# Kernel tuning notes

Measured on AMD Instinct MI355X. Metric: run time of the kernel, lower is better.

Reference implementation:

```python
import jax, jax.numpy as jnp
from jax import lax
import numpy as np

B, T, H, E = 4096, 16, 1024, 1024


def setup_inputs() -> dict:
    key = jax.random.key(0)
    ks = jax.random.split(key, 6)
    query = jax.random.normal(ks[0], (B, H), dtype=jnp.float32)
    topics = jax.random.normal(ks[1], (B, T, E), dtype=jnp.float32)
    coverage_vector = jax.random.uniform(ks[2], (B, T), dtype=jnp.float32)
    # Ua: Linear(embed->hidden, bias=False); weight [H, E]
    Ua_w = jax.random.normal(ks[3], (H, E), dtype=jnp.float32) * 0.03
    # Wa: Linear(hidden->hidden, bias=False). Applied repeatedly (T times) to
    # query in the original loop, so keep spectral norm < 1 for stability.
    Wa_w = jax.random.normal(ks[4], (H, H), dtype=jnp.float32) * 0.01
    # va: Linear(hidden->1, bias=True)
    va_w = jax.random.normal(ks[5], (1, H), dtype=jnp.float32) * 0.03
    va_b = jnp.zeros((1,), dtype=jnp.float32)
    return {"query": query, "topics": topics, "coverage_vector": coverage_vector,
            "Ua_w": Ua_w, "Wa_w": Wa_w, "va_w": va_w, "va_b": va_b}


def reference(query, topics, coverage_vector, Ua_w, Wa_w, va_w, va_b):
    # proj_key for all steps at once: Ua(topics[:, i, :]) -> [B, T, H]
    proj_keys = jnp.einsum('bte,he->bth', topics, Ua_w)
    # Original loop mutates query = Wa(query) each step, so step i uses
    # Wa^(i+1) @ query. Sequential dependence -> lax.scan over T.
    def step(q, pk_c):
        pk, c = pk_c                       # pk: [B, H], c: [B]
        q = q @ Wa_w.T                     # query = Wa(query)
        s = (jnp.tanh(q + pk) @ va_w.T)[:, 0] + va_b[0]  # va(tanh(.)) -> [B]
        return q, s * c                    # scale by coverage C_t[:, i]
    xs = (jnp.swapaxes(proj_keys, 0, 1), coverage_vector.T)  # [T,B,H], [T,B]
    _, scores = lax.scan(step, query, xs)  # scores: [T, B]
    scores = scores.T                      # [B, T]
    alphas = jax.nn.softmax(scores, axis=1)
    mt = jnp.einsum('bt,bte->be', alphas, topics)  # bmm(alphas[:,None,:], topics)
    return mt, alphas
```

## Files before the change

kernel.cpp:

```cpp
#include <hip/hip_runtime.h>

typedef unsigned short u16;
typedef unsigned int u32;
typedef __attribute__((ext_vector_type(8))) __bf16 bf16x8;
typedef __attribute__((ext_vector_type(4))) float f32x4;

__device__ __forceinline__ u16 f2bf(float f) {
  u32 u = __float_as_uint(f);
  u32 r = (u + 0x7FFFu + ((u >> 16) & 1u)) >> 16;
  return (u16)r;
}

__device__ __forceinline__ void gload_lds16(const void* g, void* l) {
  __builtin_amdgcn_global_load_lds((const __attribute__((address_space(1))) u32*)g,
                                   (__attribute__((address_space(3))) u32*)l, 16, 0, 0);
}

__device__ __forceinline__ float fast_tanh(float x) {
  x = fminf(fmaxf(x, -15.f), 15.f);
  float e2 = __expf(2.f * x);
  return (e2 - 1.f) / (e2 + 1.f);
}

__global__ __launch_bounds__(256) void cvt_kernel(const float* __restrict__ src,
                                                  u16* __restrict__ dst, int n4) {
  int stride = gridDim.x * blockDim.x;
  for (int i = blockIdx.x * blockDim.x + threadIdx.x; i < n4; i += stride) {
    float4 v = reinterpret_cast<const float4*>(src)[i];
    ushort4 o;
    o.x = f2bf(v.x); o.y = f2bf(v.y); o.z = f2bf(v.z); o.w = f2bf(v.w);
    reinterpret_cast<ushort4*>(dst)[i] = o;
  }
}

__global__ __launch_bounds__(256) void cvt3_kernel(const float* __restrict__ q_src, u16* __restrict__ q_dst,
                                                   const float* __restrict__ u_src, u16* __restrict__ u_dst,
                                                   const float* __restrict__ w_src, u16* __restrict__ w_dst) {
  int b = blockIdx.x;
  const float* src; u16* dst; int i;
  if (b < 4096)      { src = q_src; dst = q_dst; i = b * 256 + threadIdx.x; }
  else if (b < 5120) { src = u_src; dst = u_dst; i = (b - 4096) * 256 + threadIdx.x; }
  else               { src = w_src; dst = w_dst; i = (b - 5120) * 256 + threadIdx.x; }
  float4 v = reinterpret_cast<const float4*>(src)[i];
  ushort4 o;
  o.x = f2bf(v.x); o.y = f2bf(v.y); o.z = f2bf(v.z); o.w = f2bf(v.w);
  reinterpret_cast<ushort4*>(dst)[i] = o;
}

__global__ __launch_bounds__(256) void transpose_bf16_kernel(const float* __restrict__ src,
                                                             u16* __restrict__ dst) {
  __shared__ float tile[32][33];
  int tx = threadIdx.x & 31, ty = threadIdx.x >> 5;
  int bx = blockIdx.x * 32, by = blockIdx.y * 32;
#pragma unroll
  for (int j = 0; j < 32; j += 8)
    tile[ty + j][tx] = src[(size_t)(by + ty + j) * 1024 + bx + tx];
  __syncthreads();
#pragma unroll
  for (int j = 0; j < 32; j += 8)
    dst[(size_t)(bx + ty + j) * 1024 + by + tx] = f2bf(tile[tx][ty + j]);
}

__device__ __forceinline__ void stage_tile(const u16* __restrict__ g, size_t row_stride,
                                           u16* lds, int tid) {
#pragma unroll
  for (int s = 0; s < 4; ++s) {
    int chunk = s * 256 + tid;
    int row = chunk >> 3;
    int kcl = (chunk & 7) ^ (row & 7);
    const u16* gp = g + (size_t)row * row_stride + (size_t)(kcl * 8);
    u16* lp = lds + (tid >> 6) * 512 + s * 2048;
    gload_lds16(gp, lp);
  }
}

struct PowArgs {
  const u16* A[8];
  const u16* Bt[8];
  u16* C[8];
  u16* Ct[8];
};

__global__ __launch_bounds__(256) void pow_gemm_kernel(PowArgs args) {
  const u16* A  = args.A[blockIdx.z];
  const u16* Bt = args.Bt[blockIdx.z];
  u16* C  = args.C[blockIdx.z];
  u16* Ct = args.Ct[blockIdx.z];

  __shared__ __align__(16) u16 As[8192];
  __shared__ __align__(16) u16 Bs[8192];

  int tid = threadIdx.x;
  int lane = tid & 63, wave = tid >> 6;
  int wr = wave >> 1, wc = wave & 1;
  int lr = lane & 15, lg = lane >> 4;
  int m0 = blockIdx.x * 128, n0 = blockIdx.y * 128;

  f32x4 acc[4][4];
  const f32x4 zero = {0.f, 0.f, 0.f, 0.f};
#pragma unroll
  for (int m = 0; m < 4; ++m)
#pragma unroll
    for (int n = 0; n < 4; ++n) acc[m][n] = zero;

  for (int k0 = 0; k0 < 1024; k0 += 64) {
    stage_tile(A + (size_t)m0 * 1024 + k0, 1024, As, tid);
    stage_tile(Bt + (size_t)n0 * 1024 + k0, 1024, Bs, tid);
    __syncthreads();
#pragma unroll
    for (int ks = 0; ks < 2; ++ks) {
      bf16x8 a[4], b[4];
#pragma unroll
      for (int m = 0; m < 4; ++m) {
        int ra = wr * 64 + m * 16 + lr;
        a[m] = *reinterpret_cast<const bf16x8*>(As + ra * 64 + (((ks * 4 + lg) ^ (ra & 7)) << 3));
      }
#pragma unroll
      for (int n = 0; n < 4; ++n) {
        int rb = wc * 64 + n * 16 + lr;
        b[n] = *reinterpret_cast<const bf16x8*>(Bs + rb * 64 + (((ks * 4 + lg) ^ (rb & 7)) << 3));
      }
#pragma unroll
      for (int m = 0; m < 4; ++m)
#pragma unroll
        for (int n = 0; n < 4; ++n)
          acc[m][n] = __builtin_amdgcn_mfma_f32_16x16x32_bf16(a[m], b[n], acc[m][n], 0, 0, 0);
    }
    __syncthreads();
  }

#pragma unroll
  for (int m = 0; m < 4; ++m) {
    int row0 = m0 + wr * 64 + m * 16 + lg * 4;
#pragma unroll
    for (int n = 0; n < 4; ++n) {
      int col = n0 + wc * 64 + n * 16 + lr;
      f32x4 c = acc[m][n];
      ushort4 pk;
      pk.x = f2bf(c[0]); pk.y = f2bf(c[1]); pk.z = f2bf(c[2]); pk.w = f2bf(c[3]);
      C[(size_t)(row0 + 0) * 1024 + col] = pk.x;
      C[(size_t)(row0 + 1) * 1024 + col] = pk.y;
      C[(size_t)(row0 + 2) * 1024 + col] = pk.z;
      C[(size_t)(row0 + 3) * 1024 + col] = pk.w;
      *reinterpret_cast<ushort4*>(Ct + (size_t)col * 1024 + row0) = pk;
    }
  }
}

__device__ __forceinline__ void stage_tile64(const u16* __restrict__ g, u16* lds, int tid) {
#pragma unroll
  for (int s = 0; s < 2; ++s) {
    int chunk = s * 256 + tid;
    int row = chunk >> 3;
    int kcl = (chunk & 7) ^ (row & 7);
    const u16* gp = g + (size_t)row * 1024 + (size_t)(kcl * 8);
    u16* lp = lds + (tid >> 6) * 512 + s * 2048;
    gload_lds16(gp, lp);
  }
}

__global__ __launch_bounds__(256) void pow64_gemm_kernel(PowArgs args) {
  const u16* A  = args.A[blockIdx.z];
  const u16* Bt = args.Bt[blockIdx.z];
  u16* C  = args.C[blockIdx.z];
  u16* Ct = args.Ct[blockIdx.z];

  __shared__ __align__(16) u16 As[4096];
  __shared__ __align__(16) u16 Bs[4096];

  int tid = threadIdx.x;
  int lane = tid & 63, wave = tid >> 6;
  int wr = wave >> 1, wc = wave & 1;
  int lr = lane & 15, lg = lane >> 4;
  int m0 = blockIdx.x * 64, n0 = blockIdx.y * 64;

  f32x4 acc[2][2];
  const f32x4 zero = {0.f, 0.f, 0.f, 0.f};
#pragma unroll
  for (int m = 0; m < 2; ++m)
#pragma unroll
    for (int n = 0; n < 2; ++n) acc[m][n] = zero;

  for (int k0 = 0; k0 < 1024; k0 += 64) {
    stage_tile64(A + (size_t)m0 * 1024 + k0, As, tid);
    stage_tile64(Bt + (size_t)n0 * 1024 + k0, Bs, tid);
    __syncthreads();
#pragma unroll
    for (int ks = 0; ks < 2; ++ks) {
      bf16x8 a[2], b[2];
#pragma unroll
      for (int m = 0; m < 2; ++m) {
        int ra = wr * 32 + m * 16 + lr;
        a[m] = *reinterpret_cast<const bf16x8*>(As + ra * 64 + (((ks * 4 + lg) ^ (ra & 7)) << 3));
      }
#pragma unroll
      for (int n = 0; n < 2; ++n) {
        int rb = wc * 32 + n * 16 + lr;
        b[n] = *reinterpret_cast<const bf16x8*>(Bs + rb * 64 + (((ks * 4 + lg) ^ (rb & 7)) << 3));
      }
#pragma unroll
      for (int m = 0; m < 2; ++m)
#pragma unroll
        for (int n = 0; n < 2; ++n)
          acc[m][n] = __builtin_amdgcn_mfma_f32_16x16x32_bf16(a[m], b[n], acc[m][n], 0, 0, 0);
    }
    __syncthreads();
  }

#pragma unroll
  for (int m = 0; m < 2; ++m) {
    int row0 = m0 + wr * 32 + m * 16 + lg * 4;
#pragma unroll
    for (int n = 0; n < 2; ++n) {
      int col = n0 + wc * 32 + n * 16 + lr;
      f32x4 c = acc[m][n];
      ushort4 pk;
      pk.x = f2bf(c[0]); pk.y = f2bf(c[1]); pk.z = f2bf(c[2]); pk.w = f2bf(c[3]);
      C[(size_t)(row0 + 0) * 1024 + col] = pk.x;
      C[(size_t)(row0 + 1) * 1024 + col] = pk.y;
      C[(size_t)(row0 + 2) * 1024 + col] = pk.z;
      C[(size_t)(row0 + 3) * 1024 + col] = pk.w;
      *reinterpret_cast<ushort4*>(Ct + (size_t)col * 1024 + row0) = pk;
    }
  }
}


#define PHASE_READS(CUR, KS, MH)                                                     \
  { _Pragma("unroll") for (int i_ = 0; i_ < 4; ++i_)                                 \
      af[i_] = *reinterpret_cast<const bf16x8*>(lds + aoffv[(MH)*4 + i_] +           \
                                                (CUR)*32768 + (KS)*16384);           \
    if ((MH) == 0) { _Pragma("unroll") for (int n_ = 0; n_ < 4; ++n_)                \
      bfr[n_] = *reinterpret_cast<const bf16x8*>(lds + boffv[n_] +                   \
                                                 (CUR)*32768 + (KS)*16384); } }

#define PHASE_MFMA(MH)                                                               \
  { __builtin_amdgcn_s_barrier();                                                    \
    asm volatile("s_waitcnt lgkmcnt(0)" ::: "memory");                               \
    __builtin_amdgcn_sched_barrier(0);                                               \
    __builtin_amdgcn_s_setprio(1);                                                   \
    _Pragma("unroll") for (int i_ = 0; i_ < 4; ++i_)                                 \
      _Pragma("unroll") for (int n_ = 0; n_ < 4; ++n_)                               \
        acc[(MH)*4 + i_][n_] =                                                       \
            __builtin_amdgcn_mfma_f32_16x16x32_bf16(af[i_], bfr[n_], acc[(MH)*4 + i_][n_], 0, 0, 0); \
    __builtin_amdgcn_s_setprio(0); }

#define PHASE_END()                                                                  \
  { __builtin_amdgcn_s_barrier(); __builtin_amdgcn_sched_barrier(0); }

__global__ __launch_bounds__(512, 2) void score8_kernel(
    const u16* __restrict__ query_bf, const u16* __restrict__ topics_bf,
    const u16* __restrict__ F_base, const u16* __restrict__ Ua_bf,
    const float* __restrict__ va_w, float* __restrict__ scores_raw) {
  extern __shared__ __align__(16) char lds[];

  const int tid = threadIdx.x;
  const int lane = tid & 63, wave = tid >> 6;
  const int wm = wave >> 2, wn = wave & 3;
  const int lr = lane & 15, lg = lane >> 4;
  const int m0 = blockIdx.x * 256, n0 = blockIdx.y * 256;
  const int t = blockIdx.z;
  const int NT = 32;

  const u16* Ft = F_base + (size_t)t * (1024 * 1024);

  u32 aoffv[8], boffv[4];
#pragma unroll
  for (int m = 0; m < 8; ++m) {
    int row = wm * 128 + m * 16 + lr;
    aoffv[m] = row * 64 + ((lg ^ ((row >> 1) & 3)) << 4);
  }
#pragma unroll
  for (int n = 0; n < 4; ++n) {
    int row = wn * 64 + n * 16 + lr;
    boffv[n] = 65536 + row * 64 + ((lg ^ ((row >> 1) & 3)) << 4);
  }

  u32 goff1[2], goff2[2];
#pragma unroll
  for (int s = 0; s < 2; ++s) {
    int c = s * 512 + tid;
    int row = c >> 2;
    int cl = (c & 3) ^ ((row >> 1) & 3);
    goff1[s] = row * 1024 + cl * 8;
    goff2[s] = row * 16384 + cl * 8;
  }
  char* sdst = lds + (tid >> 6) * 1024;
  const u16* qbase = query_bf + (size_t)m0 * 1024;
  const u16* tbase = topics_bf + (size_t)m0 * 16384 + (size_t)t * 1024 - 1024;
  const u16* fbase = Ft + (size_t)n0 * 1024;
  const u16* ubase = Ua_bf + (size_t)n0 * 1024 - 1024;

  auto stageA = [&](int kt, int ks, int buf) {
    const u16* base = (kt < 16 ? qbase : tbase) + kt * 64 + ks * 32;
#pragma unroll
    for (int s = 0; s < 2; ++s) {
      u32 off = (kt < 16) ? goff1[s] : goff2[s];
      gload_lds16(base + off, sdst + buf * 32768 + ks * 16384 + s * 8192);
    }
  };
  auto stageB = [&](int kt, int ks, int buf) {
    const u16* base = (kt < 16 ? fbase : ubase) + kt * 64 + ks * 32;
#pragma unroll
    for (int s = 0; s < 2; ++s)
      gload_lds16(base + goff1[s], sdst + 65536 + buf * 32768 + ks * 16384 + s * 8192);
  };

  f32x4 acc[8][4];
  const f32x4 zero = {0.f, 0.f, 0.f, 0.f};
#pragma unroll
  for (int m = 0; m < 8; ++m)
#pragma unroll
    for (int n = 0; n < 4; ++n) acc[m][n] = zero;

  bf16x8 af[4], bfr[4];

  stageA(0, 0, 0); stageB(0, 0, 0);
  stageA(0, 1, 0); stageB(0, 1, 0);
  stageA(1, 0, 1); stageB(1, 0, 1);
  asm volatile("s_waitcnt vmcnt(4)" ::: "memory");
  __builtin_amdgcn_s_barrier();
  __builtin_amdgcn_sched_barrier(0);

#pragma unroll 2
  for (int kt = 0; kt < NT; ++kt) {
    int cur = kt & 1, nxt = cur ^ 1;
    PHASE_READS(cur, 0, 0);
    if (kt + 1 < NT) stageA(kt + 1, 1, nxt);
    PHASE_MFMA(0); PHASE_END();
    PHASE_READS(cur, 0, 1);
    if (kt + 1 < NT) stageB(kt + 1, 1, nxt);
    PHASE_MFMA(1); PHASE_END();
    PHASE_READS(cur, 1, 0);
    if (kt + 2 < NT) stageA(kt + 2, 0, cur);
    PHASE_MFMA(0); PHASE_END();
    PHASE_READS(cur, 1, 1);
    if (kt + 2 < NT) stageB(kt + 2, 0, cur);
    PHASE_MFMA(1);
    if (kt < NT - 2)       { asm volatile("s_waitcnt vmcnt(4)" ::: "memory"); }
    else if (kt == NT - 2) { asm volatile("s_waitcnt vmcnt(0)" ::: "memory"); }
    PHASE_END();
  }

  float va_c[4];
#pragma unroll
  for (int n = 0; n < 4; ++n) va_c[n] = va_w[n0 + wn * 64 + n * 16 + lr];

  float* sred = (float*)lds;
#pragma unroll
  for (int m = 0; m < 8; ++m) {
    float rs[4] = {0.f, 0.f, 0.f, 0.f};
#pragma unroll
    for (int n = 0; n < 4; ++n) {
      f32x4 c = acc[m][n];
      rs[0] += va_c[n] * fast_tanh(c[0]);
      rs[1] += va_c[n] * fast_tanh(c[1]);
      rs[2] += va_c[n] * fast_tanh(c[2]);
      rs[3] += va_c[n] * fast_tanh(c[3]);
    }
#pragma unroll
    for (int j = 0; j < 4; ++j) {
      float v = rs[j];
      v += __shfl_xor(v, 1);
      v += __shfl_xor(v, 2);
      v += __shfl_xor(v, 4);
      v += __shfl_xor(v, 8);
      if (lr == 0) sred[wn * 256 + wm * 128 + m * 16 + lg * 4 + j] = v;
    }
  }
  __syncthreads();
  if (tid < 256) {
    float s = sred[tid] + sred[256 + tid] + sred[512 + tid] + sred[768 + tid];
    atomicAdd(&scores_raw[(size_t)(m0 + tid) * 16 + t], s);
  }
}

__global__ __launch_bounds__(256) void softmax_mt_kernel(
    const float* __restrict__ scores_raw, const float* __restrict__ cov,
    const float* __restrict__ topics, const float* __restrict__ va_b,
    float* __restrict__ mt, float* __restrict__ alphas) {
  int b = blockIdx.x;
  int tid = threadIdx.x;
  float vb = va_b[0];
  float e[16];
  float mx = -3.4e38f;
#pragma unroll
  for (int t = 0; t < 16; ++t) {
    float s = (scores_raw[b * 16 + t] + vb) * cov[b * 16 + t];
    e[t] = s;
    mx = fmaxf(mx, s);
  }
  float sum = 0.f;
#pragma unroll
  for (int t = 0; t < 16; ++t) { e[t] = __expf(e[t] - mx); sum += e[t]; }
  float inv = 1.f / sum;
  if (tid == 0) {
#pragma unroll
    for (int t = 0; t < 16; ++t) alphas[b * 16 + t] = e[t] * inv;
  }
  const float4* tp = reinterpret_cast<const float4*>(topics + (size_t)b * 16384);
  float4 accv = {0.f, 0.f, 0.f, 0.f};
#pragma unroll
  for (int t = 0; t < 16; ++t) {
    float4 v = tp[t * 256 + tid];
    float a = e[t] * inv;
    accv.x += a * v.x; accv.y += a * v.y; accv.z += a * v.z; accv.w += a * v.w;
  }
  reinterpret_cast<float4*>(mt + (size_t)b * 1024)[tid] = accv;
}

extern "C" void kernel_launch(void* const* d_in, const int* in_sizes, int n_in,
                              void* d_out, int out_size, void* d_ws, size_t ws_size,
                              hipStream_t stream) {
  (void)in_sizes; (void)n_in; (void)out_size; (void)ws_size;
  const float* query = (const float*)d_in[0];
  const float* topics = (const float*)d_in[1];
  const float* cov   = (const float*)d_in[2];
  const float* Ua    = (const float*)d_in[3];
  const float* Wa    = (const float*)d_in[4];
  const float* va_w  = (const float*)d_in[5];
  const float* va_b  = (const float*)d_in[6];

  float* mt = (float*)d_out;
  float* alphas = mt + (size_t)4096 * 1024;

  char* ws = (char*)d_ws;
  u16* topics_bf = (u16*)(ws);
  u16* query_bf  = (u16*)(ws + (size_t)128 * 1024 * 1024);
  u16* Ua_bf     = (u16*)(ws + (size_t)136 * 1024 * 1024);
  u16* F_base    = (u16*)(ws + (size_t)138 * 1024 * 1024);
  u16* FT_base   = (u16*)(ws + (size_t)170 * 1024 * 1024);
  float* scores_raw = (float*)(ws + (size_t)202 * 1024 * 1024);

  hipFuncSetAttribute(reinterpret_cast<const void*>(score8_kernel),
                      hipFuncAttributeMaxDynamicSharedMemorySize, 131072);

  hipMemsetAsync(scores_raw, 0, (size_t)4096 * 16 * sizeof(float), stream);

  cvt_kernel<<<8192, 256, 0, stream>>>(topics, topics_bf, 16777216);
  cvt3_kernel<<<6144, 256, 0, stream>>>(query, query_bf, Ua, Ua_bf, Wa, F_base);
  transpose_bf16_kernel<<<dim3(32, 32), 256, 0, stream>>>(Wa, FT_base);

  const size_t MS = 1024 * 1024;
  auto F  = [&](int i) { return F_base + (size_t)i * MS; };
  auto FT = [&](int i) { return FT_base + (size_t)i * MS; };

  PowArgs a1{};
  a1.A[0] = F(0); a1.Bt[0] = FT(0); a1.C[0] = F(1); a1.Ct[0] = FT(1);
  pow64_gemm_kernel<<<dim3(16, 16, 1), 256, 0, stream>>>(a1);
  PowArgs a2{};
  a2.A[0] = F(1); a2.Bt[0] = FT(0); a2.C[0] = F(2); a2.Ct[0] = FT(2);
  a2.A[1] = F(1); a2.Bt[1] = FT(1); a2.C[1] = F(3); a2.Ct[1] = FT(3);
  pow64_gemm_kernel<<<dim3(16, 16, 2), 256, 0, stream>>>(a2);
  PowArgs a3{};
  for (int p = 0; p < 4; ++p) { a3.A[p] = F(3); a3.Bt[p] = FT(p); a3.C[p] = F(4 + p); a3.Ct[p] = FT(4 + p); }
  pow_gemm_kernel<<<dim3(8, 8, 4), 256, 0, stream>>>(a3);
  PowArgs a4{};
  for (int p = 0; p < 8; ++p) { a4.A[p] = F(7); a4.Bt[p] = FT(p); a4.C[p] = F(8 + p); a4.Ct[p] = FT(8 + p); }
  pow_gemm_kernel<<<dim3(8, 8, 8), 256, 0, stream>>>(a4);

  score8_kernel<<<dim3(16, 4, 16), 512, 131072, stream>>>(query_bf, topics_bf, F_base, Ua_bf,
                                                          va_w, scores_raw);
  softmax_mt_kernel<<<4096, 256, 0, stream>>>(scores_raw, cov, topics, va_b, mt, alphas);
}
```

Before: 817.8 us.

## Merge conversion kernels, remap score blocks, widen MFMA phases, drop score atomics

Folds the Wa transpose into the combined bf16 conversion kernel, which removes one launch. The score GEMM now runs on a 1D grid with a remapped block order, presumably so blocks are spread across XCDs and L2 reuse improves. Its main loop now has two phases per k-tile: each loads all 8 A fragments and issues 32 MFMAs, where before there were four half-size phases. The atomicAdd on scores is replaced by per-column-block partial buffers that the softmax kernel sums, which also removes the memset. The wider phases raise register pressure from the larger fragment array and have fewer barrier points at which to overlap staging loads.

Result: no change. 817.6 us (-0.0%).

```diff
diff --git a/kernel.cpp b/kernel.cpp
--- a/kernel.cpp
+++ b/kernel.cpp
@@ -33,32 +33,33 @@
   }
 }
 
-__global__ __launch_bounds__(256) void cvt3_kernel(const float* __restrict__ q_src, u16* __restrict__ q_dst,
-                                                   const float* __restrict__ u_src, u16* __restrict__ u_dst,
-                                                   const float* __restrict__ w_src, u16* __restrict__ w_dst) {
+__global__ __launch_bounds__(256) void cvt3t_kernel(const float* __restrict__ q_src, u16* __restrict__ q_dst,
+                                                    const float* __restrict__ u_src, u16* __restrict__ u_dst,
+                                                    const float* __restrict__ w_src, u16* __restrict__ w_dst,
+                                                    u16* __restrict__ wt_dst) {
+  __shared__ float tile[32][33];
   int b = blockIdx.x;
-  const float* src; u16* dst; int i;
-  if (b < 4096)      { src = q_src; dst = q_dst; i = b * 256 + threadIdx.x; }
-  else if (b < 5120) { src = u_src; dst = u_dst; i = (b - 4096) * 256 + threadIdx.x; }
-  else               { src = w_src; dst = w_dst; i = (b - 5120) * 256 + threadIdx.x; }
-  float4 v = reinterpret_cast<const float4*>(src)[i];
-  ushort4 o;
-  o.x = f2bf(v.x); o.y = f2bf(v.y); o.z = f2bf(v.z); o.w = f2bf(v.w);
-  reinterpret_cast<ushort4*>(dst)[i] = o;
-}
-
-__global__ __launch_bounds__(256) void transpose_bf16_kernel(const float* __restrict__ src,
-                                                             u16* __restrict__ dst) {
-  __shared__ float tile[32][33];
-  int tx = threadIdx.x & 31, ty = threadIdx.x >> 5;
-  int bx = blockIdx.x * 32, by = blockIdx.y * 32;
-#pragma unroll
-  for (int j = 0; j < 32; j += 8)
-    tile[ty + j][tx] = src[(size_t)(by + ty + j) * 1024 + bx + tx];
-  __syncthreads();
-#pragma unroll
-  for (int j = 0; j < 32; j += 8)
-    dst[(size_t)(bx + ty + j) * 1024 + by + tx] = f2bf(tile[tx][ty + j]);
+  if (b < 6144) {
+    const float* src; u16* dst; int i;
+    if (b < 4096)      { src = q_src; dst = q_dst; i = b * 256 + threadIdx.x; }
+    else if (b < 5120) { src = u_src; dst = u_dst; i = (b - 4096) * 256 + threadIdx.x; }
+    else               { src = w_src; dst = w_dst; i = (b - 5120) * 256 + threadIdx.x; }
+    float4 v = reinterpret_cast<const float4*>(src)[i];
+    ushort4 o;
+    o.x = f2bf(v.x); o.y = f2bf(v.y); o.z = f2bf(v.z); o.w = f2bf(v.w);
+    reinterpret_cast<ushort4*>(dst)[i] = o;
+  } else {
+    int tb = b - 6144;
+    int tx = threadIdx.x & 31, ty = threadIdx.x >> 5;
+    int bx = (tb & 31) * 32, by = (tb >> 5) * 32;
+#pragma unroll
+    for (int j = 0; j < 32; j += 8)
+      tile[ty + j][tx] = w_src[(size_t)(by + ty + j) * 1024 + bx + tx];
+    __syncthreads();
+#pragma unroll
+    for (int j = 0; j < 32; j += 8)
+      wt_dst[(size_t)(bx + ty + j) * 1024 + by + tx] = f2bf(tile[tx][ty + j]);
+  }
 }
 
 __device__ __forceinline__ void stage_tile(const u16* __restrict__ g, size_t row_stride,
@@ -226,40 +227,42 @@
 }
 
 
-#define PHASE_READS(CUR, KS, MH)                                                     \
-  { _Pragma("unroll") for (int i_ = 0; i_ < 4; ++i_)                                 \
-      af[i_] = *reinterpret_cast<const bf16x8*>(lds + aoffv[(MH)*4 + i_] +           \
-                                                (CUR)*32768 + (KS)*16384);           \
-    if ((MH) == 0) { _Pragma("unroll") for (int n_ = 0; n_ < 4; ++n_)                \
-      bfr[n_] = *reinterpret_cast<const bf16x8*>(lds + boffv[n_] +                   \
-                                                 (CUR)*32768 + (KS)*16384); } }
-
-#define PHASE_MFMA(MH)                                                               \
-  { __builtin_amdgcn_s_barrier();                                                    \
-    asm volatile("s_waitcnt lgkmcnt(0)" ::: "memory");                               \
-    __builtin_amdgcn_sched_barrier(0);                                               \
-    __builtin_amdgcn_s_setprio(1);                                                   \
-    _Pragma("unroll") for (int i_ = 0; i_ < 4; ++i_)                                 \
-      _Pragma("unroll") for (int n_ = 0; n_ < 4; ++n_)                               \
-        acc[(MH)*4 + i_][n_] =                                                       \
-            __builtin_amdgcn_mfma_f32_16x16x32_bf16(af[i_], bfr[n_], acc[(MH)*4 + i_][n_], 0, 0, 0); \
-    __builtin_amdgcn_s_setprio(0); }
-
-#define PHASE_END()                                                                  \
-  { __builtin_amdgcn_s_barrier(); __builtin_amdgcn_sched_barrier(0); }
+#define QPHASE(CUR, KS, STAGE_STMT, WAIT_STMT)                                        \
+  { _Pragma("unroll") for (int m_ = 0; m_ < 8; ++m_)                                  \
+      af[m_] = *reinterpret_cast<const bf16x8*>(lds + aoffv[m_] +                     \
+                                                (CUR)*32768 + (KS)*16384);            \
+    _Pragma("unroll") for (int n_ = 0; n_ < 4; ++n_)                                  \
+      bfr[n_] = *reinterpret_cast<const bf16x8*>(lds + boffv[n_] +                    \
+                                                 (CUR)*32768 + (KS)*16384);           \
+    STAGE_STMT;                                                                       \
+    __builtin_amdgcn_s_barrier();                                                     \
+    asm volatile("s_waitcnt lgkmcnt(0)" ::: "memory");                                \
+    __builtin_amdgcn_sched_barrier(0);                                                \
+    __builtin_amdgcn_s_setprio(1);                                                    \
+    _Pragma("unroll") for (int m_ = 0; m_ < 8; ++m_)                                  \
+      _Pragma("unroll") for (int n_ = 0; n_ < 4; ++n_)                                \
+        acc[m_][n_] =                                                                 \
+            __builtin_amdgcn_mfma_f32_16x16x32_bf16(af[m_], bfr[n_], acc[m_][n_], 0, 0, 0); \
+    __builtin_amdgcn_s_setprio(0);                                                    \
+    WAIT_STMT;                                                                        \
+    __builtin_amdgcn_s_barrier();                                                     \
+    __builtin_amdgcn_sched_barrier(0); }
 
 __global__ __launch_bounds__(512, 2) void score8_kernel(
     const u16* __restrict__ query_bf, const u16* __restrict__ topics_bf,
     const u16* __restrict__ F_base, const u16* __restrict__ Ua_bf,
-    const float* __restrict__ va_w, float* __restrict__ scores_raw) {
+    const float* __restrict__ va_w, float* __restrict__ scores_part) {
   extern __shared__ __align__(16) char lds[];
 
   const int tid = threadIdx.x;
   const int lane = tid & 63, wave = tid >> 6;
   const int wm = wave >> 2, wn = wave & 3;
   const int lr = lane & 15, lg = lane >> 4;
-  const int m0 = blockIdx.x * 256, n0 = blockIdx.y * 256;
-  const int t = blockIdx.z;
+
+  const int bid = blockIdx.x;
+  const int lid = (bid & 7) * 128 + (bid >> 3);
+  const int x = lid & 15, y = (lid >> 4) & 3, t = lid >> 6;
+  const int m0 = x * 256, n0 = y * 256;
   const int NT = 32;
 
   const u16* Ft = F_base + (size_t)t * (1024 * 1024);
@@ -313,7 +316,7 @@
 #pragma unroll
     for (int n = 0; n < 4; ++n) acc[m][n] = zero;
 
-  bf16x8 af[4], bfr[4];
+  bf16x8 af[8], bfr[4];
 
   stageA(0, 0, 0); stageB(0, 0, 0);
   stageA(0, 1, 0); stageB(0, 1, 0);
@@ -325,21 +328,13 @@
 #pragma unroll 2
   for (int kt = 0; kt < NT; ++kt) {
     int cur = kt & 1, nxt = cur ^ 1;
-    PHASE_READS(cur, 0, 0);
-    if (kt + 1 < NT) stageA(kt + 1, 1, nxt);
-    PHASE_MFMA(0); PHASE_END();
-    PHASE_READS(cur, 0, 1);
-    if (kt + 1 < NT) stageB(kt + 1, 1, nxt);
-    PHASE_MFMA(1); PHASE_END();
-    PHASE_READS(cur, 1, 0);
-    if (kt + 2 < NT) stageA(kt + 2, 0, cur);
-    PHASE_MFMA(0); PHASE_END();
-    PHASE_READS(cur, 1, 1);
-    if (kt + 2 < NT) stageB(kt + 2, 0, cur);
-    PHASE_MFMA(1);
-    if (kt < NT - 2)       { asm volatile("s_waitcnt vmcnt(4)" ::: "memory"); }
-    else if (kt == NT - 2) { asm volatile("s_waitcnt vmcnt(0)" ::: "memory"); }
-    PHASE_END();
+    QPHASE(cur, 0,
+           { if (kt + 1 < NT) { stageA(kt + 1, 1, nxt); stageB(kt + 1, 1, nxt); } },
+           {});
+    QPHASE(cur, 1,
+           { if (kt + 2 < NT) { stageA(kt + 2, 0, cur); stageB(kt + 2, 0, cur); } },
+           { if (kt < NT - 2)       { asm volatile("s_waitcnt vmcnt(4)" ::: "memory"); }
+             else if (kt == NT - 2) { asm volatile("s_waitcnt vmcnt(0)" ::: "memory"); } });
   }
 
   float va_c[4];
@@ -371,12 +366,12 @@
   __syncthreads();
   if (tid < 256) {
     float s = sred[tid] + sred[256 + tid] + sred[512 + tid] + sred[768 + tid];
-    atomicAdd(&scores_raw[(size_t)(m0 + tid) * 16 + t], s);
+    scores_part[((size_t)y * 4096 + m0 + tid) * 16 + t] = s;
   }
 }
 
 __global__ __launch_bounds__(256) void softmax_mt_kernel(
-    const float* __restrict__ scores_raw, const float* __restrict__ cov,
+    const float* __restrict__ scores_part, const float* __restrict__ cov,
     const float* __restrict__ topics, const float* __restrict__ va_b,
     float* __restrict__ mt, float* __restrict__ alphas) {
   int b = blockIdx.x;
@@ -386,7 +381,10 @@
   float mx = -3.4e38f;
 #pragma unroll
   for (int t = 0; t < 16; ++t) {
-    float s = (scores_raw[b * 16 + t] + vb) * cov[b * 16 + t];
+    float s = 0.f;
+#pragma unroll
+    for (int yy = 0; yy < 4; ++yy) s += scores_part[((size_t)yy * 4096 + b) * 16 + t];
+    s = (s + vb) * cov[b * 16 + t];
     e[t] = s;
     mx = fmaxf(mx, s);
   }
@@ -430,16 +428,13 @@
   u16* Ua_bf     = (u16*)(ws + (size_t)136 * 1024 * 1024);
   u16* F_base    = (u16*)(ws + (size_t)138 * 1024 * 1024);
   u16* FT_base   = (u16*)(ws + (size_t)170 * 1024 * 1024);
-  float* scores_raw = (float*)(ws + (size_t)202 * 1024 * 1024);
+  float* scores_part = (float*)(ws + (size_t)202 * 1024 * 1024);
 
   hipFuncSetAttribute(reinterpret_cast<const void*>(score8_kernel),
                       hipFuncAttributeMaxDynamicSharedMemorySize, 131072);
 
-  hipMemsetAsync(scores_raw, 0, (size_t)4096 * 16 * sizeof(float), stream);
-
   cvt_kernel<<<8192, 256, 0, stream>>>(topics, topics_bf, 16777216);
-  cvt3_kernel<<<6144, 256, 0, stream>>>(query, query_bf, Ua, Ua_bf, Wa, F_base);
-  transpose_bf16_kernel<<<dim3(32, 32), 256, 0, stream>>>(Wa, FT_base);
+  cvt3t_kernel<<<7168, 256, 0, stream>>>(query, query_bf, Ua, Ua_bf, Wa, F_base, FT_base);
 
   const size_t MS = 1024 * 1024;
   auto F  = [&](int i) { return F_base + (size_t)i * MS; };
@@ -459,7 +454,7 @@
   for (int p = 0; p < 8; ++p) { a4.A[p] = F(7); a4.Bt[p] = FT(p); a4.C[p] = F(8 + p); a4.Ct[p] = FT(8 + p); }
   pow_gemm_kernel<<<dim3(8, 8, 8), 256, 0, stream>>>(a4);
 
-  score8_kernel<<<dim3(16, 4, 16), 512, 131072, stream>>>(query_bf, topics_bf, F_base, Ua_bf,
-                                                          va_w, scores_raw);
-  softmax_mt_kernel<<<4096, 256, 0, stream>>>(scores_raw, cov, topics, va_b, mt, alphas);
-}
+  score8_kernel<<<1024, 512, 131072, stream>>>(query_bf, topics_bf, F_base, Ua_bf,
+                                               va_w, scores_part);
+  softmax_mt_kernel<<<4096, 256, 0, stream>>>(scores_part, cov, topics, va_b, mt, alphas);
+}
```
